# Kernel optimization log

Measured on AMD Instinct MI355X. Metric: run time of the kernel, lower is better.

## Reference

```python
import jax, jax.numpy as jnp
import numpy as np

B, N, D, H, K, ITERS = 32, 4096, 256, 4, 8, 3
DH = D // H
HID = 512
EPS = 1e-8
LN_EPS = 1e-5
SCALE = DH ** -0.5


def _ln(x, g, b):
    m = jnp.mean(x, axis=-1, keepdims=True)
    v = jnp.mean(jnp.square(x - m), axis=-1, keepdims=True)
    return (x - m) * jax.lax.rsqrt(v + LN_EPS) * g + b


def setup_inputs() -> dict:
    key = jax.random.key(0)
    ks = jax.random.split(key, 16)
    s = 1.0 / np.sqrt(D)
    inp = {
        "inputs": jax.random.normal(ks[0], (B, N, D), jnp.float32),
        "noise": jax.random.normal(ks[1], (B, K, D), jnp.float32),
        "slots_mu": jax.random.normal(ks[2], (1, 1, D), jnp.float32),
        "slots_logsigma": jax.random.normal(ks[3], (1, 1, D), jnp.float32) * 0.05,
        "g_in": jnp.ones((D,), jnp.float32), "b_in": jnp.zeros((D,), jnp.float32),
        "g_sl": jnp.ones((D,), jnp.float32), "b_sl": jnp.zeros((D,), jnp.float32),
        "g_ml": jnp.ones((D,), jnp.float32), "b_ml": jnp.zeros((D,), jnp.float32),
        "Wq": jax.random.normal(ks[4], (D, D), jnp.float32) * s,
        "Wk": jax.random.normal(ks[5], (D, D), jnp.float32) * s,
        "Wv": jax.random.normal(ks[6], (D, D), jnp.float32) * s,
        "Wc": jax.random.normal(ks[7], (D, D), jnp.float32) * s,
        "gru_wih": jax.random.normal(ks[8], (3 * D, D), jnp.float32) * s,
        "gru_whh": jax.random.normal(ks[9], (3 * D, D), jnp.float32) * s,
        "gru_bih": jnp.zeros((3 * D,), jnp.float32),
        "gru_bhh": jnp.zeros((3 * D,), jnp.float32),
        "W1": jax.random.normal(ks[10], (D, HID), jnp.float32) * s,
        "b1": jnp.zeros((HID,), jnp.float32),
        "W2": jax.random.normal(ks[11], (HID, D), jnp.float32) / np.sqrt(HID),
        "b2": jnp.zeros((D,), jnp.float32),
    }
    return inp


def _split(t):  # [B, n, D] -> [B, H, n, DH]
    b, n, _ = t.shape
    return t.reshape(b, n, H, DH).transpose(0, 2, 1, 3)


def reference(inputs, noise, slots_mu, slots_logsigma, g_in, b_in, g_sl, b_sl,
              g_ml, b_ml, Wq, Wk, Wv, Wc, gru_wih, gru_whh, gru_bih, gru_bhh,
              W1, b1, W2, b2):
    slots = slots_mu + jnp.exp(slots_logsigma) * noise  # [B, K, D]
    x = _ln(inputs, g_in, b_in)
    k_feat = _split(x @ Wk)  # [B, H, N, DH]
    v_feat = _split(x @ Wv)
    for _ in range(ITERS):
        slots_prev = slots
        q = _split(_ln(slots, g_sl, b_sl) @ Wq)  # [B, H, K, DH]
        dots = jnp.einsum('bhkd,bhnd->bhkn', q, k_feat) * SCALE
        attn = jax.nn.softmax(dots, axis=-2)  # competitive softmax over slots
        attn = attn / (jnp.sum(attn, axis=-1, keepdims=True) + EPS)
        upd = jnp.einsum('bhkn,bhnd->bhkd', attn, v_feat)
        upd = upd.transpose(0, 2, 1, 3).reshape(B, K, D) @ Wc  # combine heads
        # GRUCell (torch layout: rows r, z, n)
        u = upd.reshape(-1, D)
        h = slots_prev.reshape(-1, D)
        gi = u @ gru_wih.T + gru_bih
        gh = h @ gru_whh.T + gru_bhh
        r = jax.nn.sigmoid(gi[:, :D] + gh[:, :D])
        z = jax.nn.sigmoid(gi[:, D:2 * D] + gh[:, D:2 * D])
        ncand = jnp.tanh(gi[:, 2 * D:] + r * gh[:, 2 * D:])
        slots = ((1.0 - z) * ncand + z * h).reshape(B, K, D)
        slots = slots + (jax.nn.relu(_ln(slots, g_ml, b_ml) @ W1 + b1) @ W2 + b2)
    return slots
```

## Files before the change

kernel.cpp:

```cpp
#include <hip/hip_runtime.h>
#include <hip/hip_bf16.h>
#include <stdint.h>

typedef unsigned short u16;
typedef _Float16 f16;
typedef __attribute__((ext_vector_type(4))) float f32x4;
typedef __attribute__((ext_vector_type(8))) _Float16 h16x8;
typedef __attribute__((ext_vector_type(4))) _Float16 h16x4;

#define LN_EPS 1e-5f
#define ATT_EPS 1e-8f

__global__ __launch_bounds__(256) void init_slots_k(
    const float* __restrict__ noise, const float* __restrict__ mu,
    const float* __restrict__ lsig, float* __restrict__ slots)
{
  int i = blockIdx.x * 256 + threadIdx.x;
  int d = i & 255;
  slots[i] = mu[d] + __expf(lsig[d]) * noise[i];
}

__global__ __launch_bounds__(256) void prep_w_k(
    const float* __restrict__ Wk, const float* __restrict__ whh,
    f16* __restrict__ WkT16, float* __restrict__ whhT)
{
  int i = blockIdx.x * 256 + threadIdx.x;
  if (i < 65536) {
    int c = i >> 8, kd = i & 255;
    WkT16[i] = (f16)Wk[kd * 256 + c];
  }
  int d = i / 768, j = i - d * 768;
  whhT[i] = whh[j * 256 + d];
}

__global__ __launch_bounds__(256) void prep_f_k(
    const float* __restrict__ Wc, const float* __restrict__ wih,
    float* __restrict__ fihT)
{
  __shared__ float wcs[16][257];
  __shared__ float ws[32][257];
  int t = threadIdx.x;
  int d0 = blockIdx.x * 16, j0 = blockIdx.y * 32;
  for (int i = t; i < 4096; i += 256) {
    int r = i >> 8, c = i & 255;
    wcs[r][c] = Wc[(d0 + r) * 256 + c];
  }
  for (int i = t; i < 8192; i += 256) {
    int r = i >> 8, c = i & 255;
    ws[r][c] = wih[(j0 + r) * 256 + c];
  }
  __syncthreads();
  int dl = t & 15, jp = t >> 4;
  float a0 = 0.f, a1 = 0.f;
#pragma unroll 8
  for (int c = 0; c < 256; c++) {
    float wv = wcs[dl][c];
    a0 += wv * ws[jp][c];
    a1 += wv * ws[jp + 16][c];
  }
  fihT[(d0 + dl) * 768 + j0 + jp] = a0;
  fihT[(d0 + dl) * 768 + j0 + jp + 16] = a1;
}

__global__ __launch_bounds__(256) void ln_x_k(
    const float* __restrict__ inputs, const float* __restrict__ g_in,
    const float* __restrict__ b_in, f16* __restrict__ xln16)
{
  int t = threadIdx.x, w = t >> 6, l = t & 63;
  float4 gv = *(const float4*)(g_in + l * 4);
  float4 bv = *(const float4*)(b_in + l * 4);
  long row0 = (long)blockIdx.x * 64 + w * 16;
#pragma unroll 2
  for (int i = 0; i < 16; i++) {
    long r = row0 + i;
    float4 x = *(const float4*)(inputs + r * 256 + l * 4);
    float s1 = x.x + x.y + x.z + x.w;
    float s2 = x.x * x.x + x.y * x.y + x.z * x.z + x.w * x.w;
#pragma unroll
    for (int off = 1; off < 64; off <<= 1) {
      s1 += __shfl_xor(s1, off);
      s2 += __shfl_xor(s2, off);
    }
    float m = s1 * (1.f / 256.f);
    float var = s2 * (1.f / 256.f) - m * m;
    float rs = rsqrtf(var + LN_EPS);
    h16x4 o;
    o[0] = (f16)((x.x - m) * rs * gv.x + bv.x);
    o[1] = (f16)((x.y - m) * rs * gv.y + bv.y);
    o[2] = (f16)((x.z - m) * rs * gv.z + bv.z);
    o[3] = (f16)((x.w - m) * rs * gv.w + bv.w);
    *(h16x4*)(xln16 + r * 256 + l * 4) = o;
  }
}

__global__ __launch_bounds__(1024) void slot_t_k(
    const float* __restrict__ slots, const float* __restrict__ g_sl,
    const float* __restrict__ b_sl, const float* __restrict__ Wq,
    const f16* __restrict__ WkT16, f16* __restrict__ tq)
{
  __shared__ float ln[256];
  __shared__ float qs[256];
  __shared__ float part[4][256];
  __shared__ float red[8];
  int t = threadIdx.x;
  int i = blockIdx.x;
  if (t < 256) {
    float x = slots[i * 256 + t];
    float a = x, bq = x * x;
#pragma unroll
    for (int off = 32; off; off >>= 1) { a += __shfl_down(a, off); bq += __shfl_down(bq, off); }
    if ((t & 63) == 0) { red[t >> 6] = a; red[4 + (t >> 6)] = bq; }
  }
  __syncthreads();
  if (t < 256) {
    float x = slots[i * 256 + t];
    float S1 = red[0] + red[1] + red[2] + red[3];
    float S2 = red[4] + red[5] + red[6] + red[7];
    float m = S1 * (1.f / 256.f);
    float var = S2 * (1.f / 256.f) - m * m;
    float rstd = rsqrtf(var + LN_EPS);
    ln[t] = (x - m) * rstd * g_sl[t] + b_sl[t];
  }
  __syncthreads();
  int col = t & 255, ks = t >> 8;
  float acc = 0.f;
#pragma unroll 16
  for (int dd = 0; dd < 64; dd++) {
    int d = ks * 64 + dd;
    acc += ln[d] * Wq[d * 256 + col];
  }
  part[ks][col] = acc;
  __syncthreads();
  if (t < 256) qs[t] = part[0][t] + part[1][t] + part[2][t] + part[3][t];
  __syncthreads();
  int h = t >> 8, d2 = t & 255;
  float tt = 0.f;
#pragma unroll 8
  for (int dp = 0; dp < 64; dp++)
    tt += qs[h * 64 + dp] * (float)WkT16[(h * 64 + dp) * 256 + d2];
  tq[((i >> 3) * 32 + h * 8 + (i & 7)) * 256 + d2] = (f16)(tt * 0.125f);
}

__global__ __launch_bounds__(256, 3) void attn_fused_k(
    const f16* __restrict__ xln16, const f16* __restrict__ tq,
    f16* __restrict__ y_part, float* __restrict__ sums_part)
{
  __shared__ u16 xsT[256 * 64];
  __shared__ u16 attT[32 * 64];
  __shared__ float asum_s[4][32];
  int b = blockIdx.x, nc = blockIdx.y, t = threadIdx.x;
  int nb = nc * 128;
  int w = t >> 6, l = t & 63;
  int lc = l & 15, lg = l >> 4;
  h16x8 tb0[8], tb1[8];
#pragma unroll
  for (int k0 = 0; k0 < 8; k0++) {
    tb0[k0] = *(const h16x8*)(tq + (b * 32 + lc) * 256 + k0 * 32 + lg * 8);
    tb1[k0] = *(const h16x8*)(tq + (b * 32 + lc + 16) * 256 + k0 * 32 + lg * 8);
  }
  f32x4 acc0[4], acc1[4];
#pragma unroll
  for (int dt = 0; dt < 4; dt++) { acc0[dt] = (f32x4){0,0,0,0}; acc1[dt] = (f32x4){0,0,0,0}; }
  float as0 = 0.f, as1 = 0.f;

  for (int sub = 0; sub < 2; sub++) {
    __syncthreads();
    {
      int nl8 = t >> 5, dchunk = t & 31;
      const f16* gp = xln16 + ((long)(b * 4096 + nb + sub * 64 + nl8 * 8)) * 256 + dchunk * 8;
      h16x8 v0 = *(const h16x8*)(gp);
      h16x8 v1 = *(const h16x8*)(gp + 256);
      h16x8 v2 = *(const h16x8*)(gp + 512);
      h16x8 v3 = *(const h16x8*)(gp + 768);
      h16x8 v4 = *(const h16x8*)(gp + 1024);
      h16x8 v5 = *(const h16x8*)(gp + 1280);
      h16x8 v6 = *(const h16x8*)(gp + 1536);
      h16x8 v7 = *(const h16x8*)(gp + 1792);
#pragma unroll
      for (int j = 0; j < 8; j++) {
        h16x8 o;
        o[0] = v0[j]; o[1] = v1[j]; o[2] = v2[j]; o[3] = v3[j];
        o[4] = v4[j]; o[5] = v5[j]; o[6] = v6[j]; o[7] = v7[j];
        int d = dchunk * 8 + j;
        *(h16x8*)((char*)xsT + d * 128 + ((nl8 ^ j) << 4)) = o;
      }
    }
    f32x4 D0 = {0,0,0,0}, D1 = {0,0,0,0};
    {
      const f16* ga = xln16 + ((long)(b * 4096 + nb + sub * 64 + w * 16 + lc)) * 256 + lg * 8;
#pragma unroll
      for (int k0 = 0; k0 < 8; k0++) {
        h16x8 af = *(const h16x8*)(ga + k0 * 32);
        D0 = __builtin_amdgcn_mfma_f32_16x16x32_f16(af, tb0[k0], D0, 0, 0, 0);
        D1 = __builtin_amdgcn_mfma_f32_16x16x32_f16(af, tb1[k0], D1, 0, 0, 0);
      }
    }
    h16x4 pk0, pk1;
#pragma unroll
    for (int r = 0; r < 4; r++) {
      float d0 = D0[r], d1 = D1[r];
      float m0 = d0, m1 = d1;
      m0 = fmaxf(m0, __shfl_xor(m0, 1)); m0 = fmaxf(m0, __shfl_xor(m0, 2)); m0 = fmaxf(m0, __shfl_xor(m0, 4));
      m1 = fmaxf(m1, __shfl_xor(m1, 1)); m1 = fmaxf(m1, __shfl_xor(m1, 2)); m1 = fmaxf(m1, __shfl_xor(m1, 4));
      float e0 = __expf(d0 - m0), e1 = __expf(d1 - m1);
      float s0 = e0, s1 = e1;
      s0 += __shfl_xor(s0, 1); s0 += __shfl_xor(s0, 2); s0 += __shfl_xor(s0, 4);
      s1 += __shfl_xor(s1, 1); s1 += __shfl_xor(s1, 2); s1 += __shfl_xor(s1, 4);
      f16 a0h = (f16)(e0 / s0), a1h = (f16)(e1 / s1);
      as0 += (float)a0h; as1 += (float)a1h;
      pk0[r] = a0h; pk1[r] = a1h;
    }
    {
      int slot = w * 2 + (lg >> 1);
      int boff = (lg & 1) * 8;
      *(h16x4*)((char*)attT + lc * 128 + ((slot ^ (lc & 7)) << 4) + boff) = pk0;
      *(h16x4*)((char*)attT + (lc + 16) * 128 + ((slot ^ (lc & 7)) << 4) + boff) = pk1;
    }
    __syncthreads();
    h16x8 A00, A01, A10, A11;
    {
      int hs0 = lc, hs1 = 16 + lc, sw = lc & 7;
      A00 = *(const h16x8*)((char*)attT + hs0 * 128 + ((lg ^ sw) << 4));
      A01 = *(const h16x8*)((char*)attT + hs0 * 128 + (((4 + lg) ^ sw) << 4));
      A10 = *(const h16x8*)((char*)attT + hs1 * 128 + ((lg ^ sw) << 4));
      A11 = *(const h16x8*)((char*)attT + hs1 * 128 + (((4 + lg) ^ sw) << 4));
    }
#pragma unroll
    for (int dt = 0; dt < 4; dt++) {
      int d = w * 64 + dt * 16 + lc;
      h16x8 B0 = *(const h16x8*)((char*)xsT + d * 128 + ((lg ^ (d & 7)) << 4));
      h16x8 B1 = *(const h16x8*)((char*)xsT + d * 128 + (((4 + lg) ^ (d & 7)) << 4));
      acc0[dt] = __builtin_amdgcn_mfma_f32_16x16x32_f16(A00, B0, acc0[dt], 0, 0, 0);
      acc0[dt] = __builtin_amdgcn_mfma_f32_16x16x32_f16(A01, B1, acc0[dt], 0, 0, 0);
      acc1[dt] = __builtin_amdgcn_mfma_f32_16x16x32_f16(A10, B0, acc1[dt], 0, 0, 0);
      acc1[dt] = __builtin_amdgcn_mfma_f32_16x16x32_f16(A11, B1, acc1[dt], 0, 0, 0);
    }
  }
  as0 += __shfl_xor(as0, 16); as0 += __shfl_xor(as0, 32);
  as1 += __shfl_xor(as1, 16); as1 += __shfl_xor(as1, 32);
  if (l < 16) { asum_s[w][l] = as0; asum_s[w][l + 16] = as1; }
  __syncthreads();
  if (t < 32)
    sums_part[(nc * 32 + b) * 32 + t] =
        asum_s[0][t] + asum_s[1][t] + asum_s[2][t] + asum_s[3][t];
  long ybase = ((long)(nc * 32 + b) * 32) * 256;
#pragma unroll
  for (int reg = 0; reg < 4; reg++) {
    int hsA = lg * 4 + reg;
#pragma unroll
    for (int dt = 0; dt < 4; dt++) {
      int d = w * 64 + dt * 16 + lc;
      y_part[ybase + hsA * 256 + d] = (f16)acc0[dt][reg];
      y_part[ybase + (16 + hsA) * 256 + d] = (f16)acc1[dt][reg];
    }
  }
}

__global__ __launch_bounds__(1024) void combine_k(
    const f16* __restrict__ y_part, const float* __restrict__ sums_part,
    float* __restrict__ slots, const float* __restrict__ Wv,
    const float* __restrict__ fihT, const float* __restrict__ whhT,
    const float* __restrict__ bih, const float* __restrict__ bhh,
    const float* __restrict__ g_ml, const float* __restrict__ b_ml,
    const float* __restrict__ W1, const float* __restrict__ b1,
    const float* __restrict__ W2, const float* __restrict__ b2,
    const float* __restrict__ g_sl, const float* __restrict__ b_sl,
    const float* __restrict__ Wq, const f16* __restrict__ WkT16,
    f16* __restrict__ tq, int cq)
{
  __shared__ float ysn[4][256];
  __shared__ float uls[256], hls[256], sns[256], lns[256];
  __shared__ float hid[512];
  __shared__ float part2[4][256];
  __shared__ float part6[4][256][7];
  __shared__ float part5[2][512];
  __shared__ float red[8];
  int t = threadIdx.x;
  int i = blockIdx.x;
  int b = i >> 3, k = i & 7;
  {
    int j = t >> 8, d = t & 255;
    float den = ATT_EPS, yv = 0.f;
#pragma unroll 8
    for (int ncq = 0; ncq < 32; ncq++) {
      int hsrow = (ncq * 32 + b) * 32 + j * 8 + k;
      den += sums_part[hsrow];
      yv += (float)y_part[(long)hsrow * 256 + d];
    }
    ysn[j][d] = yv / den;
    if (t < 256) hls[t] = slots[i * 256 + t];
  }
  __syncthreads();
  int col = t & 255, ks = t >> 8;
  {
    int h = col >> 6;
    float acc = 0.f;
#pragma unroll 16
    for (int dd = 0; dd < 64; dd++) {
      int d = ks * 64 + dd;
      acc += ysn[h][d] * Wv[d * 256 + col];
    }
    part2[ks][col] = acc;
  }
  __syncthreads();
  if (t < 256) uls[t] = part2[0][t] + part2[1][t] + part2[2][t] + part2[3][t];
  __syncthreads();
  {
    float a0 = 0.f, a1 = 0.f, a2 = 0.f, h0 = 0.f, h1 = 0.f, h2 = 0.f;
#pragma unroll 4
    for (int dd = 0; dd < 64; dd++) {
      int d = ks * 64 + dd;
      float u = uls[d], hh = hls[d];
      const float* fi = fihT + d * 768 + col;
      const float* wh = whhT + d * 768 + col;
      a0 += u * fi[0]; a1 += u * fi[256]; a2 += u * fi[512];
      h0 += hh * wh[0]; h1 += hh * wh[256]; h2 += hh * wh[512];
    }
    part6[ks][col][0] = a0; part6[ks][col][1] = a1; part6[ks][col][2] = a2;
    part6[ks][col][3] = h0; part6[ks][col][4] = h1; part6[ks][col][5] = h2;
  }
  __syncthreads();
  if (t < 256) {
    float gi0 = part6[0][t][0] + part6[1][t][0] + part6[2][t][0] + part6[3][t][0] + bih[t];
    float gi1 = part6[0][t][1] + part6[1][t][1] + part6[2][t][1] + part6[3][t][1] + bih[256 + t];
    float gi2 = part6[0][t][2] + part6[1][t][2] + part6[2][t][2] + part6[3][t][2] + bih[512 + t];
    float gh0 = part6[0][t][3] + part6[1][t][3] + part6[2][t][3] + part6[3][t][3] + bhh[t];
    float gh1 = part6[0][t][4] + part6[1][t][4] + part6[2][t][4] + part6[3][t][4] + bhh[256 + t];
    float gh2 = part6[0][t][5] + part6[1][t][5] + part6[2][t][5] + part6[3][t][5] + bhh[512 + t];
    float r = 1.f / (1.f + __expf(-(gi0 + gh0)));
    float z = 1.f / (1.f + __expf(-(gi1 + gh1)));
    float nc2 = tanhf(gi2 + r * gh2);
    float sn = (1.f - z) * nc2 + z * hls[t];
    sns[t] = sn;
    float a = sn, bq = sn * sn;
#pragma unroll
    for (int off = 32; off; off >>= 1) { a += __shfl_down(a, off); bq += __shfl_down(bq, off); }
    if ((t & 63) == 0) { red[t >> 6] = a; red[4 + (t >> 6)] = bq; }
  }
  __syncthreads();
  if (t < 256) {
    float S1 = red[0] + red[1] + red[2] + red[3];
    float S2 = red[4] + red[5] + red[6] + red[7];
    float mean = S1 * (1.f / 256.f);
    float var = S2 * (1.f / 256.f) - mean * mean;
    float rstd = rsqrtf(var + LN_EPS);
    lns[t] = (sns[t] - mean) * rstd * g_ml[t] + b_ml[t];
  }
  __syncthreads();
  {
    int c5 = t & 511, k5 = t >> 9;
    float acc = 0.f;
#pragma unroll 16
    for (int dd = 0; dd < 128; dd++) {
      int d = k5 * 128 + dd;
      acc += lns[d] * W1[d * 512 + c5];
    }
    part5[k5][c5] = acc;
  }
  __syncthreads();
  if (t < 512) hid[t] = fmaxf(part5[0][t] + part5[1][t] + b1[t], 0.f);
  __syncthreads();
  {
    float acc = 0.f;
#pragma unroll 16
    for (int dd = 0; dd < 128; dd++) {
      int d = ks * 128 + dd;
      acc += hid[d] * W2[d * 256 + col];
    }
    part2[ks][col] = acc;
  }
  __syncthreads();
  float outv = 0.f;
  if (t < 256) {
    outv = sns[t] + b2[t] + part2[0][t] + part2[1][t] + part2[2][t] + part2[3][t];
    slots[i * 256 + t] = outv;
  }
  if (!cq) return;
  if (t < 256) {
    float a = outv, bq = outv * outv;
#pragma unroll
    for (int off = 32; off; off >>= 1) { a += __shfl_down(a, off); bq += __shfl_down(bq, off); }
    if ((t & 63) == 0) { red[t >> 6] = a; red[4 + (t >> 6)] = bq; }
  }
  __syncthreads();
  if (t < 256) {
    float S1 = red[0] + red[1] + red[2] + red[3];
    float S2 = red[4] + red[5] + red[6] + red[7];
    float mean = S1 * (1.f / 256.f);
    float var = S2 * (1.f / 256.f) - mean * mean;
    float rstd = rsqrtf(var + LN_EPS);
    lns[t] = (outv - mean) * rstd * g_sl[t] + b_sl[t];
  }
  __syncthreads();
  {
    float acc = 0.f;
#pragma unroll 16
    for (int dd = 0; dd < 64; dd++) {
      int d = ks * 64 + dd;
      acc += lns[d] * Wq[d * 256 + col];
    }
    part2[ks][col] = acc;
  }
  __syncthreads();
  if (t < 256) uls[t] = part2[0][t] + part2[1][t] + part2[2][t] + part2[3][t];
  __syncthreads();
  {
    int h2 = t >> 8, d2 = t & 255;
    float tt = 0.f;
#pragma unroll 8
    for (int dp = 0; dp < 64; dp++)
      tt += uls[h2 * 64 + dp] * (float)WkT16[(h2 * 64 + dp) * 256 + d2];
    tq[(b * 32 + h2 * 8 + k) * 256 + d2] = (f16)(tt * 0.125f);
  }
}

extern "C" void kernel_launch(void* const* d_in, const int* in_sizes, int n_in,
                              void* d_out, int out_size, void* d_ws, size_t ws_size,
                              hipStream_t stream)
{
  const float* inputs = (const float*)d_in[0];
  const float* noise  = (const float*)d_in[1];
  const float* mu     = (const float*)d_in[2];
  const float* lsig   = (const float*)d_in[3];
  const float* g_in   = (const float*)d_in[4];
  const float* b_in   = (const float*)d_in[5];
  const float* g_sl   = (const float*)d_in[6];
  const float* b_sl   = (const float*)d_in[7];
  const float* g_ml   = (const float*)d_in[8];
  const float* b_ml   = (const float*)d_in[9];
  const float* Wq     = (const float*)d_in[10];
  const float* Wk     = (const float*)d_in[11];
  const float* Wv     = (const float*)d_in[12];
  const float* Wc     = (const float*)d_in[13];
  const float* wih    = (const float*)d_in[14];
  const float* whh    = (const float*)d_in[15];
  const float* bih    = (const float*)d_in[16];
  const float* bhh    = (const float*)d_in[17];
  const float* W1     = (const float*)d_in[18];
  const float* b1     = (const float*)d_in[19];
  const float* W2     = (const float*)d_in[20];
  const float* b2     = (const float*)d_in[21];

  char* ws = (char*)d_ws;
  f16*   xln16  = (f16*)(ws);
  f16*   y_part = (f16*)(ws + 67108864);
  f16*   tq     = (f16*)(ws + 83886080);
  float* slots  = (float*)(ws + 84410368);
  float* sumsp  = (float*)(ws + 84672512);
  f16*   WkT16  = (f16*)(ws + 84803584);
  float* fihT   = (float*)(ws + 84934656);
  float* whhT   = (float*)(ws + 85721088);

  init_slots_k<<<256, 256, 0, stream>>>(noise, mu, lsig, slots);
  prep_w_k<<<768, 256, 0, stream>>>(Wk, whh, WkT16, whhT);
  prep_f_k<<<dim3(16, 24), 256, 0, stream>>>(Wc, wih, fihT);
  ln_x_k<<<2048, 256, 0, stream>>>(inputs, g_in, b_in, xln16);
  slot_t_k<<<256, 1024, 0, stream>>>(slots, g_sl, b_sl, Wq, WkT16, tq);
  for (int it = 0; it < 3; ++it) {
    attn_fused_k<<<dim3(32, 32), 256, 0, stream>>>(xln16, tq, y_part, sumsp);
    combine_k<<<256, 1024, 0, stream>>>(y_part, sumsp, slots, Wv, fihT, whhT,
                                        bih, bhh, g_ml, b_ml, W1, b1, W2, b2,
                                        g_sl, b_sl, Wq, WkT16, tq, (it < 2) ? 1 : 0);
  }
  hipMemcpyAsync(d_out, slots, 65536 * sizeof(float), hipMemcpyDeviceToDevice, stream);
}
```

Baseline: 282.4 us.

## Stage attention A-tile in LDS and vectorize combine-kernel matvecs with float4

In the attention kernel, the xln16 tile that was already loaded for the transpose is now also written to a swizzled row-major LDS buffer, and the MFMA A operand reads from there instead of issuing a second global load. This adds 32KB of shared memory and an extra barrier, so the occupancy hint drops from 3 to 2 blocks. In the combine kernel, the Wv, W1, W2 and Wq matvecs now use float4 weight loads with a wider split-K reduction through f32x4 partial buffers. That cuts load instruction count but makes the final sums longer.

Result: faster. 263.0 us (median of 2 runs) (-6.9%).

```diff
diff --git a/kernel.cpp b/kernel.cpp
--- a/kernel.cpp
+++ b/kernel.cpp
@@ -141,10 +141,11 @@
   tq[((i >> 3) * 32 + h * 8 + (i & 7)) * 256 + d2] = (f16)(tt * 0.125f);
 }
 
-__global__ __launch_bounds__(256, 3) void attn_fused_k(
+__global__ __launch_bounds__(256, 2) void attn_fused_k(
     const f16* __restrict__ xln16, const f16* __restrict__ tq,
     f16* __restrict__ y_part, float* __restrict__ sums_part)
 {
+  __shared__ u16 xs[64 * 256];
   __shared__ u16 xsT[256 * 64];
   __shared__ u16 attT[32 * 64];
   __shared__ float asum_s[4][32];
@@ -176,6 +177,17 @@
       h16x8 v5 = *(const h16x8*)(gp + 1280);
       h16x8 v6 = *(const h16x8*)(gp + 1536);
       h16x8 v7 = *(const h16x8*)(gp + 1792);
+      {
+        int r0 = nl8 * 8;
+        *(h16x8*)((char*)xs + (r0 + 0) * 512 + ((dchunk ^ ((r0 + 0) & 31)) << 4)) = v0;
+        *(h16x8*)((char*)xs + (r0 + 1) * 512 + ((dchunk ^ ((r0 + 1) & 31)) << 4)) = v1;
+        *(h16x8*)((char*)xs + (r0 + 2) * 512 + ((dchunk ^ ((r0 + 2) & 31)) << 4)) = v2;
+        *(h16x8*)((char*)xs + (r0 + 3) * 512 + ((dchunk ^ ((r0 + 3) & 31)) << 4)) = v3;
+        *(h16x8*)((char*)xs + (r0 + 4) * 512 + ((dchunk ^ ((r0 + 4) & 31)) << 4)) = v4;
+        *(h16x8*)((char*)xs + (r0 + 5) * 512 + ((dchunk ^ ((r0 + 5) & 31)) << 4)) = v5;
+        *(h16x8*)((char*)xs + (r0 + 6) * 512 + ((dchunk ^ ((r0 + 6) & 31)) << 4)) = v6;
+        *(h16x8*)((char*)xs + (r0 + 7) * 512 + ((dchunk ^ ((r0 + 7) & 31)) << 4)) = v7;
+      }
 #pragma unroll
       for (int j = 0; j < 8; j++) {
         h16x8 o;
@@ -185,12 +197,14 @@
         *(h16x8*)((char*)xsT + d * 128 + ((nl8 ^ j) << 4)) = o;
       }
     }
+    __syncthreads();
     f32x4 D0 = {0,0,0,0}, D1 = {0,0,0,0};
     {
-      const f16* ga = xln16 + ((long)(b * 4096 + nb + sub * 64 + w * 16 + lc)) * 256 + lg * 8;
+      int row = w * 16 + lc, sw = row & 31;
 #pragma unroll
       for (int k0 = 0; k0 < 8; k0++) {
-        h16x8 af = *(const h16x8*)(ga + k0 * 32);
+        int sd8 = k0 * 4 + lg;
+        h16x8 af = *(const h16x8*)((char*)xs + row * 512 + ((sd8 ^ sw) << 4));
         D0 = __builtin_amdgcn_mfma_f32_16x16x32_f16(af, tb0[k0], D0, 0, 0, 0);
         D1 = __builtin_amdgcn_mfma_f32_16x16x32_f16(af, tb1[k0], D1, 0, 0, 0);
       }
@@ -271,9 +285,9 @@
   __shared__ float ysn[4][256];
   __shared__ float uls[256], hls[256], sns[256], lns[256];
   __shared__ float hid[512];
-  __shared__ float part2[4][256];
+  __shared__ f32x4 part16[16][64];
+  __shared__ f32x4 part5q[8][128];
   __shared__ float part6[4][256][7];
-  __shared__ float part5[2][512];
   __shared__ float red[8];
   int t = threadIdx.x;
   int i = blockIdx.x;
@@ -292,18 +306,29 @@
   }
   __syncthreads();
   int col = t & 255, ks = t >> 8;
-  {
-    int h = col >> 6;
-    float acc = 0.f;
-#pragma unroll 16
-    for (int dd = 0; dd < 64; dd++) {
-      int d = ks * 64 + dd;
-      acc += ysn[h][d] * Wv[d * 256 + col];
-    }
-    part2[ks][col] = acc;
-  }
-  __syncthreads();
-  if (t < 256) uls[t] = part2[0][t] + part2[1][t] + part2[2][t] + part2[3][t];
+  int qc = t & 63, ks16 = t >> 6;
+  int col0 = qc * 4;
+  const float* p16 = (const float*)part16;
+  const float* p5 = (const float*)part5q;
+  {
+    int h = col0 >> 6;
+    f32x4 acc = {0.f, 0.f, 0.f, 0.f};
+#pragma unroll
+    for (int dd = 0; dd < 16; dd++) {
+      int d = ks16 * 16 + dd;
+      float u = ysn[h][d];
+      float4 wv = *(const float4*)(Wv + d * 256 + col0);
+      acc[0] += u * wv.x; acc[1] += u * wv.y; acc[2] += u * wv.z; acc[3] += u * wv.w;
+    }
+    part16[ks16][qc] = acc;
+  }
+  __syncthreads();
+  if (t < 256) {
+    float s = 0.f;
+#pragma unroll
+    for (int q = 0; q < 16; q++) s += p16[q * 256 + t];
+    uls[t] = s;
+  }
   __syncthreads();
   {
     float a0 = 0.f, a1 = 0.f, a2 = 0.f, h0 = 0.f, h1 = 0.f, h2 = 0.f;
@@ -348,31 +373,44 @@
   }
   __syncthreads();
   {
-    int c5 = t & 511, k5 = t >> 9;
-    float acc = 0.f;
-#pragma unroll 16
-    for (int dd = 0; dd < 128; dd++) {
-      int d = k5 * 128 + dd;
-      acc += lns[d] * W1[d * 512 + c5];
-    }
-    part5[k5][c5] = acc;
-  }
-  __syncthreads();
-  if (t < 512) hid[t] = fmaxf(part5[0][t] + part5[1][t] + b1[t], 0.f);
-  __syncthreads();
-  {
-    float acc = 0.f;
-#pragma unroll 16
-    for (int dd = 0; dd < 128; dd++) {
-      int d = ks * 128 + dd;
-      acc += hid[d] * W2[d * 256 + col];
-    }
-    part2[ks][col] = acc;
+    int qc5 = t & 127, ks8 = t >> 7;
+    int c0 = qc5 * 4;
+    f32x4 acc = {0.f, 0.f, 0.f, 0.f};
+#pragma unroll
+    for (int dd = 0; dd < 32; dd++) {
+      int d = ks8 * 32 + dd;
+      float u = lns[d];
+      float4 wv = *(const float4*)(W1 + d * 512 + c0);
+      acc[0] += u * wv.x; acc[1] += u * wv.y; acc[2] += u * wv.z; acc[3] += u * wv.w;
+    }
+    part5q[ks8][qc5] = acc;
+  }
+  __syncthreads();
+  if (t < 512) {
+    float s = 0.f;
+#pragma unroll
+    for (int q = 0; q < 8; q++) s += p5[q * 512 + t];
+    hid[t] = fmaxf(s + b1[t], 0.f);
+  }
+  __syncthreads();
+  {
+    f32x4 acc = {0.f, 0.f, 0.f, 0.f};
+#pragma unroll
+    for (int dd = 0; dd < 32; dd++) {
+      int d = ks16 * 32 + dd;
+      float u = hid[d];
+      float4 wv = *(const float4*)(W2 + d * 256 + col0);
+      acc[0] += u * wv.x; acc[1] += u * wv.y; acc[2] += u * wv.z; acc[3] += u * wv.w;
+    }
+    part16[ks16][qc] = acc;
   }
   __syncthreads();
   float outv = 0.f;
   if (t < 256) {
-    outv = sns[t] + b2[t] + part2[0][t] + part2[1][t] + part2[2][t] + part2[3][t];
+    float s = 0.f;
+#pragma unroll
+    for (int q = 0; q < 16; q++) s += p16[q * 256 + t];
+    outv = sns[t] + b2[t] + s;
     slots[i * 256 + t] = outv;
   }
   if (!cq) return;
@@ -393,16 +431,23 @@
   }
   __syncthreads();
   {
-    float acc = 0.f;
-#pragma unroll 16
-    for (int dd = 0; dd < 64; dd++) {
-      int d = ks * 64 + dd;
-      acc += lns[d] * Wq[d * 256 + col];
-    }
-    part2[ks][col] = acc;
-  }
-  __syncthreads();
-  if (t < 256) uls[t] = part2[0][t] + part2[1][t] + part2[2][t] + part2[3][t];
+    f32x4 acc = {0.f, 0.f, 0.f, 0.f};
+#pragma unroll
+    for (int dd = 0; dd < 16; dd++) {
+      int d = ks16 * 16 + dd;
+      float u = lns[d];
+      float4 wv = *(const float4*)(Wq + d * 256 + col0);
+      acc[0] += u * wv.x; acc[1] += u * wv.y; acc[2] += u * wv.z; acc[3] += u * wv.w;
+    }
+    part16[ks16][qc] = acc;
+  }
+  __syncthreads();
+  if (t < 256) {
+    float s = 0.f;
+#pragma unroll
+    for (int q = 0; q < 16; q++) s += p16[q * 256 + t];
+    uls[t] = s;
+  }
   __syncthreads();
   {
     int h2 = t >> 8, d2 = t & 255;
```
